# Kernel optimization log

Hardware: AMD Instinct MI355X
Metric: run time of the kernel (lower is better)

## Reference

```python
import jax, jax.numpy as jnp
import numpy as np

B, C, H, W = 4, 64, 128, 128
KH, KW = 5, 5
PAD = 2
HEADS, DIM_HEAD = 8, 8


def setup_inputs() -> dict:
    key = jax.random.key(0)
    k1, k2, k3, k4 = jax.random.split(key, 4)
    return {
        "features1": jax.random.normal(k1, (B, C, H, W), dtype=jnp.float32),
        "features2": jax.random.normal(k2, (B, C, H, W), dtype=jnp.float32),
        "rel_h": jax.random.normal(k3, (C // 2, 1, 1, KH, 1), dtype=jnp.float32),
        "rel_w": jax.random.normal(k4, (C // 2, 1, 1, 1, KW), dtype=jnp.float32),
    }


def reference(features1, features2, rel_h, rel_w):
    b, c, h, w = features1.shape
    K = KH * KW
    # pad key/value source spatially
    padded = jnp.pad(features2, ((0, 0), (0, 0), (PAD, PAD), (PAD, PAD)))
    # materialize sliding windows: [B, C, H, W, KH*KW], kw index minor (matches torch unfold(2).unfold(3))
    windows = jnp.stack(
        [padded[:, :, i:i + h, j:j + w] for i in range(KH) for j in range(KW)],
        axis=-1,
    )
    # relative position bias: first C/2 channels get rel_h, last C/2 get rel_w
    relh = jnp.broadcast_to(rel_h.reshape(c // 2, KH, 1), (c // 2, KH, KW))
    relw = jnp.broadcast_to(rel_w.reshape(c // 2, 1, KW), (c // 2, KH, KW))
    rel = jnp.concatenate([relh, relw], axis=0).reshape(c, K)  # [C, K]
    k = windows + rel[None, :, None, None, :]
    v = windows
    q = features1.reshape(b, HEADS, DIM_HEAD, h, w, 1)
    k = k.reshape(b, HEADS, DIM_HEAD, h, w, K)
    v = v.reshape(b, HEADS, DIM_HEAD, h, w, K)
    # per-channel windowed softmax attention (no reduction over channel in scores)
    attn = jax.nn.softmax(q * k, axis=-1)
    # einsum 'abcdef,abcdef->acbde' from torch: output is [B, dim_head, heads, H, W]
    out = jnp.einsum('bhcxyk,bhcxyk->bchxy', attn, v)
    return out.reshape(b, c, h, w)
```

## Files before the change

kernel.cpp:

```cpp
#include <hip/hip_runtime.h>

#define B_ 4
#define C_ 64
#define H_ 128
#define W_ 128
#define LOG2E 1.44269504088896340736f

typedef float v2f __attribute__((ext_vector_type(2)));

__device__ __forceinline__ v2f exp2v(v2f x) {
    return (v2f){ __builtin_amdgcn_exp2f(x.x), __builtin_amdgcn_exp2f(x.y) };
}

template<int HALF>
__device__ __forceinline__ void sa_body(int x0, int y0,
    const float* __restrict__ f1p, const float* __restrict__ f2p,
    const float* __restrict__ relp, float* __restrict__ outp)
{
    float rel5[5];
    #pragma unroll
    for (int k = 0; k < 5; ++k) rel5[k] = relp[k];

    const float mL = (x0 > 0) ? 1.0f : 0.0f;
    const float mR = (x0 < W_ - 4) ? 1.0f : 0.0f;
    const int eM = (x0 >= 4) ? x0 - 4 : 0;
    const int eP = (x0 <= W_ - 8) ? x0 + 4 : W_ - 4;

    float w[6][8];
    #pragma unroll
    for (int t = 0; t < 6; ++t) {
        const int ky = y0 + t - 2;
        const int kycl = ky < 0 ? 0 : (ky > H_ - 1 ? H_ - 1 : ky);
        const float rv = ((unsigned)ky < (unsigned)H_) ? 1.0f : 0.0f;
        const float* rp = f2p + kycl * W_;
        const float4 qm = *(const float4*)(rp + eM);
        const float4 q0 = *(const float4*)(rp + x0);
        const float4 qp = *(const float4*)(rp + eP);
        const float mLr = mL * rv, mRr = mR * rv;
        w[t][0] = qm.z * mLr; w[t][1] = qm.w * mLr;
        w[t][2] = q0.x * rv;  w[t][3] = q0.y * rv;
        w[t][4] = q0.z * rv;  w[t][5] = q0.w * rv;
        w[t][6] = qp.x * mRr; w[t][7] = qp.y * mRr;
    }
    const float4 qrow[2] = { *(const float4*)(f1p + y0 * W_ + x0),
                             *(const float4*)(f1p + (y0 + 1) * W_ + x0) };

    #pragma unroll
    for (int r = 0; r < 2; ++r) {
        const float qs[4] = {qrow[r].x, qrow[r].y, qrow[r].z, qrow[r].w};
        float res[4];

        #pragma unroll
        for (int xo = 0; xo < 4; ++xo) {
            const float q2 = qs[xo] * LOG2E;
            const v2f q2v = {q2, q2};

            float pr[5];
            #pragma unroll
            for (int k = 0; k < 5; ++k) pr[k] = q2 * rel5[k];
            const v2f prA = {pr[0], pr[1]};
            const v2f prB = {pr[2], pr[3]};
            const float prC = pr[4];

            v2f s0 = {0.f, 0.f}, s1 = {0.f, 0.f};
            v2f d0 = {0.f, 0.f}, d1 = {0.f, 0.f};
            float lv[5];

            #pragma unroll
            for (int i = 0; i < 5; ++i) {
                const float* W8 = w[r + i];
                const v2f va = {W8[xo + 0], W8[xo + 1]};
                const v2f vb = {W8[xo + 2], W8[xo + 3]};
                const v2f pa = (HALF == 0) ? (v2f){pr[i], pr[i]} : prA;
                const v2f pb = (HALF == 0) ? (v2f){pr[i], pr[i]} : prB;
                const v2f p0 = exp2v(__builtin_elementwise_fma(va, q2v, pa));
                s0 += p0; d0 = __builtin_elementwise_fma(p0, va, d0);
                const v2f p1 = exp2v(__builtin_elementwise_fma(vb, q2v, pb));
                s1 += p1; d1 = __builtin_elementwise_fma(p1, vb, d1);
                lv[i] = W8[xo + 4];
            }
            {
                const v2f v  = {lv[0], lv[1]};
                const v2f pp = (HALF == 0) ? (v2f){pr[0], pr[1]} : (v2f){prC, prC};
                const v2f p  = exp2v(__builtin_elementwise_fma(v, q2v, pp));
                s0 += p; d0 = __builtin_elementwise_fma(p, v, d0);
            }
            {
                const v2f v  = {lv[2], lv[3]};
                const v2f pp = (HALF == 0) ? (v2f){pr[2], pr[3]} : (v2f){prC, prC};
                const v2f p  = exp2v(__builtin_elementwise_fma(v, q2v, pp));
                s1 += p; d1 = __builtin_elementwise_fma(p, v, d1);
            }
            float ss, ds;
            {
                const float pp = (HALF == 0) ? pr[4] : prC;
                const float p  = __builtin_amdgcn_exp2f(__builtin_fmaf(q2, lv[4], pp));
                ss = p; ds = p * lv[4];
            }
            const v2f st = s0 + s1, dt = d0 + d1;
            res[xo] = (dt.x + dt.y + ds) * __builtin_amdgcn_rcpf(st.x + st.y + ss);
        }

        *(float4*)(outp + (y0 + r) * W_ + x0) = (float4){res[0], res[1], res[2], res[3]};
    }
}

__global__ __launch_bounds__(256) void sa_kernel(
    const float* __restrict__ f1, const float* __restrict__ f2,
    const float* __restrict__ relh, const float* __restrict__ relw,
    float* __restrict__ out)
{
    const int tid = threadIdx.x;
    const int xq  = tid & 31;
    const int ys  = tid >> 5;
    const int blk = blockIdx.x;
    const int by  = blk & 7;
    const int bc  = blk >> 3;
    const int c   = bc & (C_ - 1);
    const int b   = bc >> 6;
    const int x0  = xq << 2;
    const int y0  = by * 16 + ys * 2;

    const size_t img = (size_t)(b * C_ + c) * (H_ * W_);
    const float* f1p = f1 + img;
    const float* f2p = f2 + img;

    const int c_out = (c & 7) * 8 + (c >> 3);
    float* outp = out + (size_t)(b * C_ + c_out) * (H_ * W_);

    if (c < C_ / 2) sa_body<0>(x0, y0, f1p, f2p, relh + c * 5, outp);
    else            sa_body<1>(x0, y0, f1p, f2p, relw + (c - C_ / 2) * 5, outp);
}

extern "C" void kernel_launch(void* const* d_in, const int* in_sizes, int n_in,
                              void* d_out, int out_size, void* d_ws, size_t ws_size,
                              hipStream_t stream) {
    const float* f1   = (const float*)d_in[0];
    const float* f2   = (const float*)d_in[1];
    const float* relh = (const float*)d_in[2];
    const float* relw = (const float*)d_in[3];
    float* out = (float*)d_out;

    const int grid = B_ * C_ * 8;
    sa_kernel<<<grid, 256, 0, stream>>>(f1, f2, relh, relw, out);
}
```

Measured before the change: 22.53 us.

## Stage padded feature halo in LDS and remap threads to column strips

Each block now covers 8 rows of one channel image. It cooperatively loads the needed 12 padded rows of features2 into shared memory, with zero borders for padding. Each thread then computes 4 vertically adjacent outputs in one column, reading its 5x5 window from LDS. Before, each thread computed a 2x4 tile and issued redundant overlapping global float4 loads with masking. The change removes redundant global traffic and mask arithmetic, but adds a barrier, LDS bank traffic, scalar output stores and twice as many blocks.

```diff
diff --git a/kernel.cpp b/kernel.cpp
--- a/kernel.cpp
+++ b/kernel.cpp
@@ -4,6 +4,10 @@
 #define C_ 64
 #define H_ 128
 #define W_ 128
+#define R_ 4
+#define BROWS 8
+#define LROWS 12
+#define LPITCH 136
 #define LOG2E 1.44269504088896340736f
 
 typedef float v2f __attribute__((ext_vector_type(2)));
@@ -13,95 +17,66 @@
 }
 
 template<int HALF>
-__device__ __forceinline__ void sa_body(int x0, int y0,
-    const float* __restrict__ f1p, const float* __restrict__ f2p,
-    const float* __restrict__ relp, float* __restrict__ outp)
+__device__ __forceinline__ void sa_strip(
+    const float* __restrict__ lp,
+    const float* __restrict__ f1p, const float* __restrict__ relp,
+    float* __restrict__ outp, int x, int y0)
 {
     float rel5[5];
     #pragma unroll
     for (int k = 0; k < 5; ++k) rel5[k] = relp[k];
 
-    const float mL = (x0 > 0) ? 1.0f : 0.0f;
-    const float mR = (x0 < W_ - 4) ? 1.0f : 0.0f;
-    const int eM = (x0 >= 4) ? x0 - 4 : 0;
-    const int eP = (x0 <= W_ - 8) ? x0 + 4 : W_ - 4;
-
-    float w[6][8];
+    float q2[R_];
     #pragma unroll
-    for (int t = 0; t < 6; ++t) {
-        const int ky = y0 + t - 2;
-        const int kycl = ky < 0 ? 0 : (ky > H_ - 1 ? H_ - 1 : ky);
-        const float rv = ((unsigned)ky < (unsigned)H_) ? 1.0f : 0.0f;
-        const float* rp = f2p + kycl * W_;
-        const float4 qm = *(const float4*)(rp + eM);
-        const float4 q0 = *(const float4*)(rp + x0);
-        const float4 qp = *(const float4*)(rp + eP);
-        const float mLr = mL * rv, mRr = mR * rv;
-        w[t][0] = qm.z * mLr; w[t][1] = qm.w * mLr;
-        w[t][2] = q0.x * rv;  w[t][3] = q0.y * rv;
-        w[t][4] = q0.z * rv;  w[t][5] = q0.w * rv;
-        w[t][6] = qp.x * mRr; w[t][7] = qp.y * mRr;
-    }
-    const float4 qrow[2] = { *(const float4*)(f1p + y0 * W_ + x0),
-                             *(const float4*)(f1p + (y0 + 1) * W_ + x0) };
+    for (int r = 0; r < R_; ++r) q2[r] = f1p[(y0 + r) * W_ + x] * LOG2E;
 
     #pragma unroll
-    for (int r = 0; r < 2; ++r) {
-        const float qs[4] = {qrow[r].x, qrow[r].y, qrow[r].z, qrow[r].w};
-        float res[4];
+    for (int r = 0; r < R_; ++r) {
+        const float q = q2[r];
+        const v2f qv = {q, q};
+        float pr[5];
+        #pragma unroll
+        for (int k = 0; k < 5; ++k) pr[k] = q * rel5[k];
+        const v2f prA = {pr[0], pr[1]};
+        const v2f prB = {pr[2], pr[3]};
+        const float prC = pr[4];
+
+        v2f s0 = {0.f,0.f}, s1 = {0.f,0.f}, d0 = {0.f,0.f}, d1 = {0.f,0.f};
+        float lv[5];
 
         #pragma unroll
-        for (int xo = 0; xo < 4; ++xo) {
-            const float q2 = qs[xo] * LOG2E;
-            const v2f q2v = {q2, q2};
-
-            float pr[5];
-            #pragma unroll
-            for (int k = 0; k < 5; ++k) pr[k] = q2 * rel5[k];
-            const v2f prA = {pr[0], pr[1]};
-            const v2f prB = {pr[2], pr[3]};
-            const float prC = pr[4];
-
-            v2f s0 = {0.f, 0.f}, s1 = {0.f, 0.f};
-            v2f d0 = {0.f, 0.f}, d1 = {0.f, 0.f};
-            float lv[5];
-
-            #pragma unroll
-            for (int i = 0; i < 5; ++i) {
-                const float* W8 = w[r + i];
-                const v2f va = {W8[xo + 0], W8[xo + 1]};
-                const v2f vb = {W8[xo + 2], W8[xo + 3]};
-                const v2f pa = (HALF == 0) ? (v2f){pr[i], pr[i]} : prA;
-                const v2f pb = (HALF == 0) ? (v2f){pr[i], pr[i]} : prB;
-                const v2f p0 = exp2v(__builtin_elementwise_fma(va, q2v, pa));
-                s0 += p0; d0 = __builtin_elementwise_fma(p0, va, d0);
-                const v2f p1 = exp2v(__builtin_elementwise_fma(vb, q2v, pb));
-                s1 += p1; d1 = __builtin_elementwise_fma(p1, vb, d1);
-                lv[i] = W8[xo + 4];
-            }
-            {
-                const v2f v  = {lv[0], lv[1]};
-                const v2f pp = (HALF == 0) ? (v2f){pr[0], pr[1]} : (v2f){prC, prC};
-                const v2f p  = exp2v(__builtin_elementwise_fma(v, q2v, pp));
-                s0 += p; d0 = __builtin_elementwise_fma(p, v, d0);
-            }
-            {
-                const v2f v  = {lv[2], lv[3]};
-                const v2f pp = (HALF == 0) ? (v2f){pr[2], pr[3]} : (v2f){prC, prC};
-                const v2f p  = exp2v(__builtin_elementwise_fma(v, q2v, pp));
-                s1 += p; d1 = __builtin_elementwise_fma(p, v, d1);
-            }
-            float ss, ds;
-            {
-                const float pp = (HALF == 0) ? pr[4] : prC;
-                const float p  = __builtin_amdgcn_exp2f(__builtin_fmaf(q2, lv[4], pp));
-                ss = p; ds = p * lv[4];
-            }
-            const v2f st = s0 + s1, dt = d0 + d1;
-            res[xo] = (dt.x + dt.y + ds) * __builtin_amdgcn_rcpf(st.x + st.y + ss);
+        for (int i = 0; i < 5; ++i) {
+            const float* row = lp + (r + i) * LPITCH;
+            const v2f va = {row[0], row[1]};
+            const v2f vb = {row[2], row[3]};
+            lv[i] = row[4];
+            const v2f pa = (HALF == 0) ? (v2f){pr[i], pr[i]} : prA;
+            const v2f pb = (HALF == 0) ? (v2f){pr[i], pr[i]} : prB;
+            const v2f p0 = exp2v(__builtin_elementwise_fma(va, qv, pa));
+            s0 += p0; d0 = __builtin_elementwise_fma(p0, va, d0);
+            const v2f p1 = exp2v(__builtin_elementwise_fma(vb, qv, pb));
+            s1 += p1; d1 = __builtin_elementwise_fma(p1, vb, d1);
         }
-
-        *(float4*)(outp + (y0 + r) * W_ + x0) = (float4){res[0], res[1], res[2], res[3]};
+        {
+            const v2f v  = {lv[0], lv[1]};
+            const v2f pp = (HALF == 0) ? (v2f){pr[0], pr[1]} : (v2f){prC, prC};
+            const v2f p  = exp2v(__builtin_elementwise_fma(v, qv, pp));
+            s0 += p; d0 = __builtin_elementwise_fma(p, v, d0);
+        }
+        {
+            const v2f v  = {lv[2], lv[3]};
+            const v2f pp = (HALF == 0) ? (v2f){pr[2], pr[3]} : (v2f){prC, prC};
+            const v2f p  = exp2v(__builtin_elementwise_fma(v, qv, pp));
+            s1 += p; d1 = __builtin_elementwise_fma(p, v, d1);
+        }
+        float ss, ds;
+        {
+            const float pp = (HALF == 0) ? pr[4] : prC;
+            const float p  = __builtin_amdgcn_exp2f(__builtin_fmaf(q, lv[4], pp));
+            ss = p; ds = p * lv[4];
+        }
+        const v2f st = s0 + s1, dt = d0 + d1;
+        outp[(y0 + r) * W_ + x] = (dt.x + dt.y + ds) * __builtin_amdgcn_rcpf(st.x + st.y + ss);
     }
 }
 
@@ -110,26 +85,46 @@
     const float* __restrict__ relh, const float* __restrict__ relw,
     float* __restrict__ out)
 {
+    __shared__ float lds[LROWS][LPITCH];
+
     const int tid = threadIdx.x;
-    const int xq  = tid & 31;
-    const int ys  = tid >> 5;
     const int blk = blockIdx.x;
-    const int by  = blk & 7;
-    const int bc  = blk >> 3;
+    const int yb  = blk & (H_ / BROWS - 1);
+    const int bc  = blk >> 4;
     const int c   = bc & (C_ - 1);
     const int b   = bc >> 6;
-    const int x0  = xq << 2;
-    const int y0  = by * 16 + ys * 2;
+    const int ybase = yb * BROWS;
 
     const size_t img = (size_t)(b * C_ + c) * (H_ * W_);
     const float* f1p = f1 + img;
     const float* f2p = f2 + img;
 
+    #pragma unroll
+    for (int k = 0; k < 3; ++k) {
+        const int idx = tid + k * 256;
+        const int row = idx >> 6;
+        const int cx  = (idx & 63) * 2;
+        const int gy  = ybase + row - 2;
+        float2 val = {0.f, 0.f};
+        if ((unsigned)gy < (unsigned)H_) val = *(const float2*)(f2p + gy * W_ + cx);
+        *(float2*)&lds[row][2 + cx] = val;
+    }
+    if (tid < 2 * LROWS) {
+        const int row = tid >> 1;
+        *(float2*)&lds[row][(tid & 1) ? 130 : 0] = (float2){0.f, 0.f};
+    }
+    __syncthreads();
+
+    const int x  = tid & (W_ - 1);
+    const int s  = tid >> 7;
+    const int y0 = ybase + s * R_;
+    const float* lp = &lds[s * R_][x];
+
     const int c_out = (c & 7) * 8 + (c >> 3);
     float* outp = out + (size_t)(b * C_ + c_out) * (H_ * W_);
 
-    if (c < C_ / 2) sa_body<0>(x0, y0, f1p, f2p, relh + c * 5, outp);
-    else            sa_body<1>(x0, y0, f1p, f2p, relw + (c - C_ / 2) * 5, outp);
+    if (c < C_ / 2) sa_strip<0>(lp, f1p, relh + c * 5, outp, x, y0);
+    else            sa_strip<1>(lp, f1p, relw + (c - C_ / 2) * 5, outp, x, y0);
 }
 
 extern "C" void kernel_launch(void* const* d_in, const int* in_sizes, int n_in,
@@ -141,6 +136,6 @@
     const float* relw = (const float*)d_in[3];
     float* out = (float*)d_out;
 
-    const int grid = B_ * C_ * 8;
+    const int grid = B_ * C_ * (H_ / BROWS);
     sa_kernel<<<grid, 256, 0, stream>>>(f1, f2, relh, relw, out);
 }
```

Result: no change. 22.72 us (+0.8%).
